# Optimization experiments

Measured on AMD Instinct MI355X. Metric: run time of the kernel, lower is better.

The kernel has to match this reference:

```python
import jax, jax.numpy as jnp
import numpy as np

H = 16
N_JOBS = 1000000
N_MACH = 500000
NEG = -1e8

PARAM_SHAPES = [("jW1",(H,H)),("jb1",(H,)),("jW2",(H,H)),("jb2",(H,)),
                ("mW1",(H,H)),("mb1",(H,)),("mW2",(H,H)),("mb2",(H,)),
                ("aj_Wq",(H,H)),("aj_bq",(H,)),("aj_Wr",(H,H)),("aj_V",(H,)),
                ("am_Wq",(H,H)),("am_bq",(H,)),("am_Wr",(H,H)),("am_V",(H,)),
                ("ja_Wq",(H,H)),("ja_bq",(H,)),("ja_Wr",(H,H)),("ja_V",(H,)),
                ("ma_Wq",(H,H)),("ma_bq",(H,)),("ma_Wr",(H,H)),("ma_V",(H,)),
                ("g1W",(H,3*H)),("g1b",(H,)),("g2W",(H,3*H)),("g2b",(H,)),
                ("last_j",(H,))]

def setup_inputs() -> dict:
    key = jax.random.key(0)
    inp = {}
    inp["jobs"] = jax.random.normal(jax.random.fold_in(key, 0), (N_JOBS, H), dtype=jnp.float32)
    inp["machines"] = jax.random.normal(jax.random.fold_in(key, 1), (N_MACH, H), dtype=jnp.float32)
    inp["alloc_jobs_mask"] = jax.random.randint(jax.random.fold_in(key, 2), (N_JOBS,), 0, 2) > 0
    for i, (name, shape) in enumerate(PARAM_SHAPES):
        inp[name] = jax.random.normal(jax.random.fold_in(key, 10 + i), shape, dtype=jnp.float32) * 0.05
    return inp

def _emb(x, W1, b1, W2, b2):
    # custom_embedding: two tanh MLP layers (torch Linear: x @ W.T + b)
    h = jnp.tanh(x @ W1.T + b1)
    return jnp.tanh(h @ W2.T + b2)

def _att_logits(q, ref, Wq, bq, Wr, V):
    # Bahdanau additive attention: tanh(W_q q + W_r ref) @ V -> [S]
    return jnp.tanh((q @ Wq.T + bq) + ref @ Wr.T) @ V

def _query_att(q, ref, Wq, bq, Wr, V):
    # Attention with use_softmax=True followed by weighted sum over ref
    w = jax.nn.softmax(_att_logits(q, ref, Wq, bq, Wr, V))
    return w @ ref  # [H]

def reference(jobs, machines, alloc_jobs_mask,
              jW1, jb1, jW2, jb2, mW1, mb1, mW2, mb2,
              aj_Wq, aj_bq, aj_Wr, aj_V, am_Wq, am_bq, am_Wr, am_V,
              ja_Wq, ja_bq, ja_Wr, ja_V, ma_Wq, ma_bq, ma_Wr, ma_V,
              g1W, g1b, g2W, g2b, last_j):
    E_j = _emb(jobs, jW1, jb1, jW2, jb2)        # [Sj, H]
    E_m = _emb(machines, mW1, mb1, mW2, mb2)    # [Sm, H]

    # glimpse 1 conditioned on last_j
    g_j1 = _query_att(last_j, E_j, aj_Wq, aj_bq, aj_Wr, aj_V)
    g_m1 = _query_att(last_j, E_m, am_Wq, am_bq, am_Wr, am_V)
    g1 = jnp.tanh(jnp.concatenate([last_j, g_j1, g_m1]) @ g1W.T + g1b)

    # job pointer logits + invalid-action masking
    j_logits = _att_logits(g1, E_j, ja_Wq, ja_bq, ja_Wr, ja_V)
    j_logits = jnp.where(alloc_jobs_mask, j_logits, NEG)
    sel_j = jnp.argmax(j_logits)
    e_js = E_j[sel_j]

    # glimpse 2 conditioned on selected job embedding
    g_j2 = _query_att(e_js, E_j, aj_Wq, aj_bq, aj_Wr, aj_V)
    g_m2 = _query_att(e_js, E_m, am_Wq, am_bq, am_Wr, am_V)
    g2 = jnp.tanh(jnp.concatenate([e_js, g_j2, g_m2]) @ g2W.T + g2b)

    m_logits = _att_logits(g2, E_m, ma_Wq, ma_bq, ma_Wr, ma_V)
    sel_m = jnp.argmax(m_logits)

    logpas = jax.nn.log_softmax(j_logits)[sel_j] + jax.nn.log_softmax(m_logits)[sel_m]
    return sel_j, sel_m, logpas
```

## Files before the change

kernel.cpp:

```cpp
#include <hip/hip_runtime.h>
#include <cstddef>
#include <cstdint>


constexpr int NJ = 1000000;
constexpr int NM = 500000;
constexpr float NEGV = -1e8f;

constexpr int BLK = 256;
constexpr int ROWS_PER_BLK = 512;
constexpr int GB_J2 = (NJ + ROWS_PER_BLK - 1) / ROWS_PER_BLK;
constexpr int GB_M2 = (NM + ROWS_PER_BLK - 1) / ROWS_PER_BLK;
constexpr int GB_TOT2 = GB_J2 + GB_M2;
constexpr int EBLK = ROWS_PER_BLK * 16;

constexpr int S_QKJA = 0;
constexpr int S_QK2J = 16;
constexpr int S_QK2M = 32;
constexpr int S_EJS  = 48;
constexpr int S_QKMA = 64;
constexpr int S_LOGPJ = 80;
constexpr int S_SELJ  = 81;
constexpr int P1J = 128;
constexpr int P1M = P1J + GB_J2 * 17;
constexpr int P2V = P1M + GB_M2 * 17;
constexpr int P2I = P2V + GB_J2;
constexpr int P2L = P2I + GB_J2;
constexpr size_t E_OFF = 65536;
static_assert(P2L + GB_J2 <= (int)E_OFF, "partials overflow into E cache");

typedef float v2f __attribute__((ext_vector_type(2)));

struct Params {
    const float *jobs, *machines;
    const int *mask;
    const float *jW1, *jb1, *jW2, *jb2;
    const float *mW1, *mb1, *mW2, *mb2;
    const float *aj_Wq, *aj_bq, *aj_Wr, *aj_V;
    const float *am_Wq, *am_bq, *am_Wr, *am_V;
    const float *ja_Wq, *ja_bq, *ja_Wr, *ja_V;
    const float *ma_Wq, *ma_bq, *ma_Wr, *ma_V;
    const float *g1W, *g1b, *g2W, *g2b, *last_j;
    float *S;
    float *Ej, *Em;
    float *out;
};


__device__ __forceinline__ float fast_tanh(float x) {
    float e = __builtin_amdgcn_exp2f(x * 2.8853900817779268f);
    float r = __builtin_amdgcn_rcpf(e + 1.0f);
    return fmaf(-2.0f, r, 1.0f);
}

__device__ __forceinline__ v2f vbc(float a) { v2f r; r.x = a; r.y = a; return r; }

__device__ __forceinline__ v2f vfma(float w, v2f b, v2f c) {
    return __builtin_elementwise_fma(vbc(w), b, c);
}
__device__ __forceinline__ v2f vfma2(v2f a, v2f b, v2f c) {
    return __builtin_elementwise_fma(a, b, c);
}
__device__ __forceinline__ v2f vtanh(v2f a) {
    v2f r; r.x = fast_tanh(a.x); r.y = fast_tanh(a.y); return r;
}

__device__ __forceinline__ void load16(const float* __restrict__ X, size_t r, float (&x)[16]) {
    const float4* p4 = reinterpret_cast<const float4*>(X) + r * 4;
    float4 a = p4[0], b = p4[1], c = p4[2], d = p4[3];
    x[0]=a.x; x[1]=a.y; x[2]=a.z; x[3]=a.w;
    x[4]=b.x; x[5]=b.y; x[6]=b.z; x[7]=b.w;
    x[8]=c.x; x[9]=c.y; x[10]=c.z; x[11]=c.w;
    x[12]=d.x; x[13]=d.y; x[14]=d.z; x[15]=d.w;
}

__device__ __forceinline__ void load16_v2(const float* __restrict__ X, size_t rA, size_t rB,
                                          v2f (&x)[16]) {
    float a[16], b[16];
    load16(X, rA, a);
    load16(X, rB, b);
#pragma unroll
    for (int k = 0; k < 16; ++k) { x[k].x = a[k]; x[k].y = b[k]; }
}

__device__ __forceinline__ void ecache_store(float* __restrict__ Eb, int t, const v2f (&e)[16]) {
    float4* p4 = reinterpret_cast<float4*>(Eb);
#pragma unroll
    for (int kp = 0; kp < 8; ++kp)
        p4[kp * 256 + t] = make_float4(e[2*kp].x, e[2*kp].y, e[2*kp+1].x, e[2*kp+1].y);
}
__device__ __forceinline__ void ecache_load(const float* __restrict__ Eb, int t, v2f (&e)[16]) {
    const float4* p4 = reinterpret_cast<const float4*>(Eb);
#pragma unroll
    for (int kp = 0; kp < 8; ++kp) {
        float4 q = p4[kp * 256 + t];
        e[2*kp].x = q.x;   e[2*kp].y = q.y;
        e[2*kp+1].x = q.z; e[2*kp+1].y = q.w;
    }
}

__device__ __forceinline__ void emb16_v2(const v2f (&x)[16],
                                         const float* __restrict__ W1, const float* __restrict__ b1,
                                         const float* __restrict__ W2, const float* __restrict__ b2,
                                         v2f (&e)[16]) {
    v2f h[16];
#pragma unroll
    for (int i = 0; i < 16; ++i) {
        v2f a = vbc(b1[i]);
#pragma unroll
        for (int k = 0; k < 16; ++k) a = vfma(W1[i * 16 + k], x[k], a);
        h[i] = vtanh(a);
    }
#pragma unroll
    for (int i = 0; i < 16; ++i) {
        v2f a = vbc(b2[i]);
#pragma unroll
        for (int k = 0; k < 16; ++k) a = vfma(W2[i * 16 + k], h[k], a);
        e[i] = vtanh(a);
    }
}

__device__ __forceinline__ v2f att_logit_v2(const v2f (&e)[16], const float (&qk)[16],
                                            const float* __restrict__ Wr,
                                            const float* __restrict__ V) {
    v2f acc = vbc(0.0f);
#pragma unroll
    for (int i = 0; i < 16; ++i) {
        v2f r = vbc(qk[i]);
#pragma unroll
        for (int k = 0; k < 16; ++k) r = vfma(Wr[i * 16 + k], e[k], r);
        acc = vfma2(vbc(V[i]), vtanh(r), acc);
    }
    return acc;
}

__device__ __forceinline__ float wave_reduce_sum(float v) {
#pragma unroll
    for (int off = 32; off > 0; off >>= 1) v += __shfl_xor(v, off, 64);
    return v;
}

__device__ __forceinline__ void wave_reduce_argmax(float &v, int &idx) {
#pragma unroll
    for (int off = 32; off > 0; off >>= 1) {
        float ov = __shfl_xor(v, off, 64);
        int oi = __shfl_xor(idx, off, 64);
        if (ov > v || (ov == v && oi < idx)) { v = ov; idx = oi; }
    }
}

__device__ __forceinline__ float block_sum(float v) {
    __shared__ float sm[4];
    v = wave_reduce_sum(v);
    __syncthreads();
    if ((threadIdx.x & 63) == 0) sm[threadIdx.x >> 6] = v;
    __syncthreads();
    return sm[0] + sm[1] + sm[2] + sm[3];
}

__device__ __forceinline__ void block_argmax(float &v, int &i) {
    __shared__ float sv[4];
    __shared__ int si[4];
    wave_reduce_argmax(v, i);
    __syncthreads();
    if ((threadIdx.x & 63) == 0) { sv[threadIdx.x >> 6] = v; si[threadIdx.x >> 6] = i; }
    __syncthreads();
    float bv = sv[0]; int bi = si[0];
#pragma unroll
    for (int k = 1; k < 4; ++k)
        if (sv[k] > bv || (sv[k] == bv && si[k] < bi)) { bv = sv[k]; bi = si[k]; }
    v = bv; i = bi;
}

__device__ __forceinline__ void block_sum17(float l, float (&s)[16], float* dst) {
    l = wave_reduce_sum(l);
#pragma unroll
    for (int i = 0; i < 16; ++i) s[i] = wave_reduce_sum(s[i]);
    __shared__ float red[4][17];
    int w = threadIdx.x >> 6, ln = threadIdx.x & 63;
    __syncthreads();
    if (ln == 0) {
        red[w][0] = l;
#pragma unroll
        for (int i = 0; i < 16; ++i) red[w][1 + i] = s[i];
    }
    __syncthreads();
    if (threadIdx.x < 17)
        dst[threadIdx.x] = red[0][threadIdx.x] + red[1][threadIdx.x] + red[2][threadIdx.x] + red[3][threadIdx.x];
}

template <bool CACHE>
__global__ __launch_bounds__(BLK) void k_emb_g1(Params p) {
    const bool isJob = blockIdx.x < GB_J2;
    const float* X  = isJob ? p.jobs : p.machines;
    const float* W1 = isJob ? p.jW1 : p.mW1;
    const float* b1 = isJob ? p.jb1 : p.mb1;
    const float* W2 = isJob ? p.jW2 : p.mW2;
    const float* b2 = isJob ? p.jb2 : p.mb2;
    const float* Wr = isJob ? p.aj_Wr : p.am_Wr;
    const float* V  = isJob ? p.aj_V  : p.am_V;
    float* E = isJob ? p.Ej : p.Em;
    const int n  = isJob ? NJ : NM;
    const int b0 = isJob ? (int)blockIdx.x : (int)blockIdx.x - GB_J2;

    __shared__ float qks[16];
    if (threadIdx.x < 16) {
        const float* Wq = isJob ? p.aj_Wq : p.am_Wq;
        const float* bq = isJob ? p.aj_bq : p.am_bq;
        const int i = threadIdx.x;
        float a = bq[i];
#pragma unroll
        for (int k = 0; k < 16; ++k) a = fmaf(Wq[i * 16 + k], p.last_j[k], a);
        qks[i] = a;
    }
    __syncthreads();
    float qk[16];
#pragma unroll
    for (int i = 0; i < 16; ++i) qk[i] = qks[i];

    const int r0 = b0 * ROWS_PER_BLK + 2 * (int)threadIdx.x;
    const int r1 = r0 + 1;
    const bool v0 = r0 < n, v1 = r1 < n;
    const size_t a0 = (size_t)(v0 ? r0 : 0);
    const size_t a1 = (size_t)(v1 ? r1 : 0);

    v2f x[16], e[16];
    load16_v2(X, a0, a1, x);
    emb16_v2(x, W1, b1, W2, b2, e);
    if (CACHE) ecache_store(E + (size_t)b0 * EBLK, (int)threadIdx.x, e);
    v2f lg = att_logit_v2(e, qk, Wr, V);
    float pw0 = v0 ? __expf(lg.x) : 0.0f;
    float pw1 = v1 ? __expf(lg.y) : 0.0f;
    float l = pw0 + pw1, s[16];
#pragma unroll
    for (int i = 0; i < 16; ++i) s[i] = fmaf(pw0, e[i].x, pw1 * e[i].y);

    block_sum17(l, s, p.S + (isJob ? P1J : P1M) + (size_t)b0 * 17);
}

__global__ __launch_bounds__(BLK) void k_combine_g(Params p, int phase) {
    const float* PJ = p.S + P1J;
    const float* PM = p.S + P1M;
    float lJ = 0.0f, lM = 0.0f, sJ[16], sM[16];
#pragma unroll
    for (int c = 0; c < 16; ++c) { sJ[c] = 0.0f; sM[c] = 0.0f; }
    for (int i = threadIdx.x; i < GB_J2; i += BLK) {
        lJ += PJ[i * 17];
#pragma unroll
        for (int c = 0; c < 16; ++c) sJ[c] += PJ[i * 17 + 1 + c];
    }
    for (int i = threadIdx.x; i < GB_M2; i += BLK) {
        lM += PM[i * 17];
#pragma unroll
        for (int c = 0; c < 16; ++c) sM[c] += PM[i * 17 + 1 + c];
    }
    __shared__ float totJ[17], totM[17];
    block_sum17(lJ, sJ, totJ);
    block_sum17(lM, sM, totM);
    __syncthreads();

    __shared__ float cb[48], gbuf[16];
    if (threadIdx.x < 16) {
        int i = threadIdx.x;
        cb[i]      = phase ? p.S[S_EJS + i] : p.last_j[i];
        cb[16 + i] = totJ[1 + i] / totJ[0];
        cb[32 + i] = totM[1 + i] / totM[0];
    }
    __syncthreads();
    const float* gW  = phase ? p.g2W : p.g1W;
    const float* gbv = phase ? p.g2b : p.g1b;
    if (threadIdx.x < 16) {
        int i = threadIdx.x;
        float a = gbv[i];
#pragma unroll
        for (int k = 0; k < 48; ++k) a = fmaf(gW[i * 48 + k], cb[k], a);
        gbuf[i] = fast_tanh(a);
    }
    __syncthreads();
    const float* Wq = phase ? p.ma_Wq : p.ja_Wq;
    const float* bq = phase ? p.ma_bq : p.ja_bq;
    const int off = phase ? S_QKMA : S_QKJA;
    if (threadIdx.x < 16) {
        int i = threadIdx.x;
        float a = bq[i];
#pragma unroll
        for (int k = 0; k < 16; ++k) a = fmaf(Wq[i * 16 + k], gbuf[k], a);
        p.S[off + i] = a;
    }
}

template <bool CACHE>
__global__ __launch_bounds__(BLK) void k_jlogits(Params p) {
    float qk[16];
#pragma unroll
    for (int i = 0; i < 16; ++i) qk[i] = p.S[S_QKJA + i];

    const int r0 = blockIdx.x * ROWS_PER_BLK + 2 * (int)threadIdx.x;
    const int r1 = r0 + 1;
    const bool v0 = r0 < NJ, v1 = r1 < NJ;
    const size_t a0 = (size_t)(v0 ? r0 : 0);
    const size_t a1 = (size_t)(v1 ? r1 : 0);

    v2f e[16];
    if (CACHE) {
        ecache_load(p.Ej + (size_t)blockIdx.x * EBLK, (int)threadIdx.x, e);
    } else {
        v2f x[16];
        load16_v2(p.jobs, a0, a1, x);
        emb16_v2(x, p.jW1, p.jb1, p.jW2, p.jb2, e);
    }
    v2f lg = att_logit_v2(e, qk, p.ja_Wr, p.ja_V);
    const bool m0 = v0 && (p.mask[a0] != 0);
    const bool m1 = v1 && (p.mask[a1] != 0);
    float l = (m0 ? __expf(lg.x) : 0.0f) + (m1 ? __expf(lg.y) : 0.0f);
    float am0 = m0 ? lg.x : NEGV - 1.0f;
    float am1 = m1 ? lg.y : NEGV - 1.0f;
    float best;
    int bi;
    if (am0 >= am1) { best = am0; bi = r0; }
    else            { best = am1; bi = r1; }

    l = wave_reduce_sum(l);
    wave_reduce_argmax(best, bi);
    __shared__ float rl[4], rv[4];
    __shared__ int ri[4];
    int w = threadIdx.x >> 6, ln = threadIdx.x & 63;
    if (ln == 0) { rl[w] = l; rv[w] = best; ri[w] = bi; }
    __syncthreads();
    if (threadIdx.x == 0) {
        float L = rl[0] + rl[1] + rl[2] + rl[3];
        float v = rv[0]; int i = ri[0];
#pragma unroll
        for (int k = 1; k < 4; ++k)
            if (rv[k] > v || (rv[k] == v && ri[k] < i)) { v = rv[k]; i = ri[k]; }
        p.S[P2V + blockIdx.x] = v;
        p.S[P2I + blockIdx.x] = (float)i;
        p.S[P2L + blockIdx.x] = L;
    }
}

__global__ __launch_bounds__(BLK) void k_combine2(Params p) {
    float v = -3.4e38f; int vi = 0x7fffffff; float l = 0.0f;
    for (int i = threadIdx.x; i < GB_J2; i += BLK) {
        float pv = p.S[P2V + i];
        int pi = (int)p.S[P2I + i];
        if (pv > v || (pv == v && pi < vi)) { v = pv; vi = pi; }
        l += p.S[P2L + i];
    }
    l = block_sum(l);
    block_argmax(v, vi);
    const int sel = vi;

    __shared__ float xb[16], hb[16], eb[16];
    if (threadIdx.x < 16) xb[threadIdx.x] = p.jobs[(size_t)sel * 16 + threadIdx.x];
    __syncthreads();
    if (threadIdx.x < 16) {
        int i = threadIdx.x;
        float a = p.jb1[i];
#pragma unroll
        for (int k = 0; k < 16; ++k) a = fmaf(p.jW1[i * 16 + k], xb[k], a);
        hb[i] = fast_tanh(a);
    }
    __syncthreads();
    if (threadIdx.x < 16) {
        int i = threadIdx.x;
        float a = p.jb2[i];
#pragma unroll
        for (int k = 0; k < 16; ++k) a = fmaf(p.jW2[i * 16 + k], hb[k], a);
        float e = fast_tanh(a);
        eb[i] = e;
        p.S[S_EJS + i] = e;
    }
    __syncthreads();
    if (threadIdx.x < 16) {
        int i = threadIdx.x;
        float a1 = p.aj_bq[i], a2 = p.am_bq[i];
#pragma unroll
        for (int k = 0; k < 16; ++k) {
            a1 = fmaf(p.aj_Wq[i * 16 + k], eb[k], a1);
            a2 = fmaf(p.am_Wq[i * 16 + k], eb[k], a2);
        }
        p.S[S_QK2J + i] = a1;
        p.S[S_QK2M + i] = a2;
    }
    if (threadIdx.x == 0) {
        p.S[S_LOGPJ] = v - logf(l);
        p.S[S_SELJ] = (float)sel;
    }
}

template <bool CACHE>
__global__ __launch_bounds__(BLK) void k_glimpse2(Params p) {
    const bool isJob = blockIdx.x < GB_J2;
    const float* Wr = isJob ? p.aj_Wr : p.am_Wr;
    const float* V  = isJob ? p.aj_V  : p.am_V;
    const float* E  = isJob ? p.Ej : p.Em;
    const float* X  = isJob ? p.jobs : p.machines;
    const float* W1 = isJob ? p.jW1 : p.mW1;
    const float* b1 = isJob ? p.jb1 : p.mb1;
    const float* W2 = isJob ? p.jW2 : p.mW2;
    const float* b2 = isJob ? p.jb2 : p.mb2;
    const int n  = isJob ? NJ : NM;
    const int b0 = isJob ? (int)blockIdx.x : (int)blockIdx.x - GB_J2;
    const int qoff = isJob ? S_QK2J : S_QK2M;

    float qk[16];
#pragma unroll
    for (int i = 0; i < 16; ++i) qk[i] = p.S[qoff + i];

    const int r0 = b0 * ROWS_PER_BLK + 2 * (int)threadIdx.x;
    const int r1 = r0 + 1;
    const bool v0 = r0 < n, v1 = r1 < n;
    const size_t a0 = (size_t)(v0 ? r0 : 0);
    const size_t a1 = (size_t)(v1 ? r1 : 0);

    v2f e[16];
    if (CACHE) {
        ecache_load(E + (size_t)b0 * EBLK, (int)threadIdx.x, e);
    } else {
        v2f x[16];
        load16_v2(X, a0, a1, x);
        emb16_v2(x, W1, b1, W2, b2, e);
    }
    v2f lg = att_logit_v2(e, qk, Wr, V);
    float pw0 = v0 ? __expf(lg.x) : 0.0f;
    float pw1 = v1 ? __expf(lg.y) : 0.0f;
    float l = pw0 + pw1, s[16];
#pragma unroll
    for (int i = 0; i < 16; ++i) s[i] = fmaf(pw0, e[i].x, pw1 * e[i].y);

    block_sum17(l, s, p.S + (isJob ? P1J : P1M) + (size_t)b0 * 17);
}

template <bool CACHE>
__global__ __launch_bounds__(BLK) void k_mlogits(Params p) {
    float qk[16];
#pragma unroll
    for (int i = 0; i < 16; ++i) qk[i] = p.S[S_QKMA + i];

    const int r0 = blockIdx.x * ROWS_PER_BLK + 2 * (int)threadIdx.x;
    const int r1 = r0 + 1;
    const bool v0 = r0 < NM, v1 = r1 < NM;
    const size_t a0 = (size_t)(v0 ? r0 : 0);
    const size_t a1 = (size_t)(v1 ? r1 : 0);

    v2f e[16];
    if (CACHE) {
        ecache_load(p.Em + (size_t)blockIdx.x * EBLK, (int)threadIdx.x, e);
    } else {
        v2f x[16];
        load16_v2(p.machines, a0, a1, x);
        emb16_v2(x, p.mW1, p.mb1, p.mW2, p.mb2, e);
    }
    v2f lg = att_logit_v2(e, qk, p.ma_Wr, p.ma_V);
    float l = (v0 ? __expf(lg.x) : 0.0f) + (v1 ? __expf(lg.y) : 0.0f);
    float am0 = v0 ? lg.x : -3.4e38f;
    float am1 = v1 ? lg.y : -3.4e38f;
    float best;
    int bi;
    if (am0 >= am1) { best = am0; bi = r0; }
    else            { best = am1; bi = r1; }

    l = wave_reduce_sum(l);
    wave_reduce_argmax(best, bi);
    __shared__ float rl[4], rv[4];
    __shared__ int ri[4];
    int w = threadIdx.x >> 6, ln = threadIdx.x & 63;
    if (ln == 0) { rl[w] = l; rv[w] = best; ri[w] = bi; }
    __syncthreads();
    if (threadIdx.x == 0) {
        float L = rl[0] + rl[1] + rl[2] + rl[3];
        float v = rv[0]; int i = ri[0];
#pragma unroll
        for (int k = 1; k < 4; ++k)
            if (rv[k] > v || (rv[k] == v && ri[k] < i)) { v = rv[k]; i = ri[k]; }
        p.S[P2V + blockIdx.x] = v;
        p.S[P2I + blockIdx.x] = (float)i;
        p.S[P2L + blockIdx.x] = L;
    }
}

__global__ __launch_bounds__(BLK) void k_combine4(Params p) {
    float v = -3.4e38f; int vi = 0x7fffffff; float l = 0.0f;
    for (int i = threadIdx.x; i < GB_M2; i += BLK) {
        float pv = p.S[P2V + i];
        int pi = (int)p.S[P2I + i];
        if (pv > v || (pv == v && pi < vi)) { v = pv; vi = pi; }
        l += p.S[P2L + i];
    }
    l = block_sum(l);
    block_argmax(v, vi);
    if (threadIdx.x == 0) {
        p.out[0] = p.S[S_SELJ];
        p.out[1] = (float)vi;
        p.out[2] = p.S[S_LOGPJ] + (v - logf(l));
    }
}

extern "C" void kernel_launch(void* const* d_in, const int* in_sizes, int n_in,
                              void* d_out, int out_size, void* d_ws, size_t ws_size,
                              hipStream_t stream) {
    Params p;
    p.jobs     = (const float*)d_in[0];
    p.machines = (const float*)d_in[1];
    p.mask     = (const int*)d_in[2];
    p.jW1 = (const float*)d_in[3];  p.jb1 = (const float*)d_in[4];
    p.jW2 = (const float*)d_in[5];  p.jb2 = (const float*)d_in[6];
    p.mW1 = (const float*)d_in[7];  p.mb1 = (const float*)d_in[8];
    p.mW2 = (const float*)d_in[9];  p.mb2 = (const float*)d_in[10];
    p.aj_Wq = (const float*)d_in[11]; p.aj_bq = (const float*)d_in[12];
    p.aj_Wr = (const float*)d_in[13]; p.aj_V  = (const float*)d_in[14];
    p.am_Wq = (const float*)d_in[15]; p.am_bq = (const float*)d_in[16];
    p.am_Wr = (const float*)d_in[17]; p.am_V  = (const float*)d_in[18];
    p.ja_Wq = (const float*)d_in[19]; p.ja_bq = (const float*)d_in[20];
    p.ja_Wr = (const float*)d_in[21]; p.ja_V  = (const float*)d_in[22];
    p.ma_Wq = (const float*)d_in[23]; p.ma_bq = (const float*)d_in[24];
    p.ma_Wr = (const float*)d_in[25]; p.ma_V  = (const float*)d_in[26];
    p.g1W = (const float*)d_in[27]; p.g1b = (const float*)d_in[28];
    p.g2W = (const float*)d_in[29]; p.g2b = (const float*)d_in[30];
    p.last_j = (const float*)d_in[31];
    p.S = (float*)d_ws;
    p.Ej = (float*)d_ws + E_OFF;
    p.Em = p.Ej + (size_t)GB_J2 * EBLK;
    p.out = (float*)d_out;

    const size_t needed = (E_OFF + (size_t)GB_TOT2 * EBLK) * sizeof(float);
    const bool cache = ws_size >= needed;

    if (cache) {
        k_emb_g1<true><<<GB_TOT2, BLK, 0, stream>>>(p);
        k_combine_g<<<1, BLK, 0, stream>>>(p, 0);
        k_jlogits<true><<<GB_J2, BLK, 0, stream>>>(p);
        k_combine2<<<1, BLK, 0, stream>>>(p);
        k_glimpse2<true><<<GB_TOT2, BLK, 0, stream>>>(p);
        k_combine_g<<<1, BLK, 0, stream>>>(p, 1);
        k_mlogits<true><<<GB_M2, BLK, 0, stream>>>(p);
        k_combine4<<<1, BLK, 0, stream>>>(p);
    } else {
        k_emb_g1<false><<<GB_TOT2, BLK, 0, stream>>>(p);
        k_combine_g<<<1, BLK, 0, stream>>>(p, 0);
        k_jlogits<false><<<GB_J2, BLK, 0, stream>>>(p);
        k_combine2<<<1, BLK, 0, stream>>>(p);
        k_glimpse2<false><<<GB_TOT2, BLK, 0, stream>>>(p);
        k_combine_g<<<1, BLK, 0, stream>>>(p, 1);
        k_mlogits<false><<<GB_M2, BLK, 0, stream>>>(p);
        k_combine4<<<1, BLK, 0, stream>>>(p);
    }
}
```

Measured before the change: 304.7 us.

## Recompute embeddings in every sweep instead of caching them, use transposed block reduction

Drops the workspace cache of the job and machine embeddings. Each of the four sweeps now reloads the raw inputs and recomputes the two-layer tanh MLP, trading extra ALU work for less memory traffic: the raw 16-float rows are the same size as the cached ones, but the large cache write in the first sweep goes away. The 17-value block reduction now uses a transpose-style butterfly, so each lane ends up holding one channel sum and far fewer shuffles are issued. The mask is read with a single int2 load, and validity is checked per pair, which assumes the row counts are even.

```diff
diff --git a/kernel.cpp b/kernel.cpp
--- a/kernel.cpp
+++ b/kernel.cpp
@@ -12,7 +12,6 @@
 constexpr int GB_J2 = (NJ + ROWS_PER_BLK - 1) / ROWS_PER_BLK;
 constexpr int GB_M2 = (NM + ROWS_PER_BLK - 1) / ROWS_PER_BLK;
 constexpr int GB_TOT2 = GB_J2 + GB_M2;
-constexpr int EBLK = ROWS_PER_BLK * 16;
 
 constexpr int S_QKJA = 0;
 constexpr int S_QK2J = 16;
@@ -26,8 +25,6 @@
 constexpr int P2V = P1M + GB_M2 * 17;
 constexpr int P2I = P2V + GB_J2;
 constexpr int P2L = P2I + GB_J2;
-constexpr size_t E_OFF = 65536;
-static_assert(P2L + GB_J2 <= (int)E_OFF, "partials overflow into E cache");
 
 typedef float v2f __attribute__((ext_vector_type(2)));
 
@@ -42,7 +39,6 @@
     const float *ma_Wq, *ma_bq, *ma_Wr, *ma_V;
     const float *g1W, *g1b, *g2W, *g2b, *last_j;
     float *S;
-    float *Ej, *Em;
     float *out;
 };
 
@@ -83,22 +79,6 @@
     for (int k = 0; k < 16; ++k) { x[k].x = a[k]; x[k].y = b[k]; }
 }
 
-__device__ __forceinline__ void ecache_store(float* __restrict__ Eb, int t, const v2f (&e)[16]) {
-    float4* p4 = reinterpret_cast<float4*>(Eb);
-#pragma unroll
-    for (int kp = 0; kp < 8; ++kp)
-        p4[kp * 256 + t] = make_float4(e[2*kp].x, e[2*kp].y, e[2*kp+1].x, e[2*kp+1].y);
-}
-__device__ __forceinline__ void ecache_load(const float* __restrict__ Eb, int t, v2f (&e)[16]) {
-    const float4* p4 = reinterpret_cast<const float4*>(Eb);
-#pragma unroll
-    for (int kp = 0; kp < 8; ++kp) {
-        float4 q = p4[kp * 256 + t];
-        e[2*kp].x = q.x;   e[2*kp].y = q.y;
-        e[2*kp+1].x = q.z; e[2*kp+1].y = q.w;
-    }
-}
-
 __device__ __forceinline__ void emb16_v2(const v2f (&x)[16],
                                          const float* __restrict__ W1, const float* __restrict__ b1,
                                          const float* __restrict__ W2, const float* __restrict__ b2,
@@ -172,25 +152,52 @@
     v = bv; i = bi;
 }
 
-__device__ __forceinline__ void block_sum17(float l, float (&s)[16], float* dst) {
-    l = wave_reduce_sum(l);
-#pragma unroll
-    for (int i = 0; i < 16; ++i) s[i] = wave_reduce_sum(s[i]);
+__device__ __forceinline__ void block_sum17(float l, const float (&s)[16], float* dst) {
+    const int lane = threadIdx.x & 63;
+    float c[8];
+#pragma unroll
+    for (int j = 0; j < 8; ++j) {
+        const bool hi = lane & 1;
+        float t = __shfl_xor(hi ? s[j] : s[j + 8], 1, 64);
+        c[j] = (hi ? s[j + 8] : s[j]) + t;
+    }
+    float d[4];
+#pragma unroll
+    for (int j = 0; j < 4; ++j) {
+        const bool hi = lane & 2;
+        float t = __shfl_xor(hi ? c[j] : c[j + 4], 2, 64);
+        d[j] = (hi ? c[j + 4] : c[j]) + t;
+    }
+    float e2[2];
+#pragma unroll
+    for (int j = 0; j < 2; ++j) {
+        const bool hi = lane & 4;
+        float t = __shfl_xor(hi ? d[j] : d[j + 2], 4, 64);
+        e2[j] = (hi ? d[j + 2] : d[j]) + t;
+    }
+    float f;
+    {
+        const bool hi = lane & 8;
+        float t = __shfl_xor(hi ? e2[0] : e2[1], 8, 64);
+        f = (hi ? e2[1] : e2[0]) + t;
+    }
+    f += __shfl_xor(f, 16, 64);
+    f += __shfl_xor(f, 32, 64);
+#pragma unroll
+    for (int off = 32; off > 0; off >>= 1) l += __shfl_xor(l, off, 64);
+
+    const int idx = ((lane & 1) << 3) | ((lane & 2) << 1) | ((lane & 4) >> 1) | ((lane & 8) >> 3);
     __shared__ float red[4][17];
-    int w = threadIdx.x >> 6, ln = threadIdx.x & 63;
-    __syncthreads();
-    if (ln == 0) {
-        red[w][0] = l;
-#pragma unroll
-        for (int i = 0; i < 16; ++i) red[w][1 + i] = s[i];
-    }
+    const int w = threadIdx.x >> 6;
+    __syncthreads();
+    if (lane < 16) red[w][1 + idx] = f;
+    if (lane == 0) red[w][0] = l;
     __syncthreads();
     if (threadIdx.x < 17)
         dst[threadIdx.x] = red[0][threadIdx.x] + red[1][threadIdx.x] + red[2][threadIdx.x] + red[3][threadIdx.x];
 }
 
-template <bool CACHE>
-__global__ __launch_bounds__(BLK) void k_emb_g1(Params p) {
+__global__ __launch_bounds__(BLK) void k_sweepA(Params p) {
     const bool isJob = blockIdx.x < GB_J2;
     const float* X  = isJob ? p.jobs : p.machines;
     const float* W1 = isJob ? p.jW1 : p.mW1;
@@ -199,7 +206,6 @@
     const float* b2 = isJob ? p.jb2 : p.mb2;
     const float* Wr = isJob ? p.aj_Wr : p.am_Wr;
     const float* V  = isJob ? p.aj_V  : p.am_V;
-    float* E = isJob ? p.Ej : p.Em;
     const int n  = isJob ? NJ : NM;
     const int b0 = isJob ? (int)blockIdx.x : (int)blockIdx.x - GB_J2;
 
@@ -219,18 +225,16 @@
     for (int i = 0; i < 16; ++i) qk[i] = qks[i];
 
     const int r0 = b0 * ROWS_PER_BLK + 2 * (int)threadIdx.x;
-    const int r1 = r0 + 1;
-    const bool v0 = r0 < n, v1 = r1 < n;
-    const size_t a0 = (size_t)(v0 ? r0 : 0);
-    const size_t a1 = (size_t)(v1 ? r1 : 0);
+    const bool v = r0 < n;
+    const size_t a0 = (size_t)(v ? r0 : 0);
+    const size_t a1 = a0 + (v ? 1 : 0);
 
     v2f x[16], e[16];
     load16_v2(X, a0, a1, x);
     emb16_v2(x, W1, b1, W2, b2, e);
-    if (CACHE) ecache_store(E + (size_t)b0 * EBLK, (int)threadIdx.x, e);
     v2f lg = att_logit_v2(e, qk, Wr, V);
-    float pw0 = v0 ? __expf(lg.x) : 0.0f;
-    float pw1 = v1 ? __expf(lg.y) : 0.0f;
+    float pw0 = v ? __expf(lg.x) : 0.0f;
+    float pw1 = v ? __expf(lg.y) : 0.0f;
     float l = pw0 + pw1, s[16];
 #pragma unroll
     for (int i = 0; i < 16; ++i) s[i] = fmaf(pw0, e[i].x, pw1 * e[i].y);
@@ -289,36 +293,32 @@
     }
 }
 
-template <bool CACHE>
-__global__ __launch_bounds__(BLK) void k_jlogits(Params p) {
+__global__ __launch_bounds__(BLK) void k_sweepB(Params p) {
     float qk[16];
 #pragma unroll
     for (int i = 0; i < 16; ++i) qk[i] = p.S[S_QKJA + i];
 
     const int r0 = blockIdx.x * ROWS_PER_BLK + 2 * (int)threadIdx.x;
-    const int r1 = r0 + 1;
-    const bool v0 = r0 < NJ, v1 = r1 < NJ;
-    const size_t a0 = (size_t)(v0 ? r0 : 0);
-    const size_t a1 = (size_t)(v1 ? r1 : 0);
-
-    v2f e[16];
-    if (CACHE) {
-        ecache_load(p.Ej + (size_t)blockIdx.x * EBLK, (int)threadIdx.x, e);
-    } else {
-        v2f x[16];
-        load16_v2(p.jobs, a0, a1, x);
-        emb16_v2(x, p.jW1, p.jb1, p.jW2, p.jb2, e);
-    }
+    const bool v = r0 < NJ;
+    const size_t a0 = (size_t)(v ? r0 : 0);
+    const size_t a1 = a0 + (v ? 1 : 0);
+
+    v2f x[16], e[16];
+    load16_v2(p.jobs, a0, a1, x);
+    emb16_v2(x, p.jW1, p.jb1, p.jW2, p.jb2, e);
     v2f lg = att_logit_v2(e, qk, p.ja_Wr, p.ja_V);
-    const bool m0 = v0 && (p.mask[a0] != 0);
-    const bool m1 = v1 && (p.mask[a1] != 0);
+
+    int2 mq = make_int2(0, 0);
+    if (v) mq = *reinterpret_cast<const int2*>(p.mask + r0);
+    const bool m0 = v && (mq.x != 0);
+    const bool m1 = v && (mq.y != 0);
     float l = (m0 ? __expf(lg.x) : 0.0f) + (m1 ? __expf(lg.y) : 0.0f);
     float am0 = m0 ? lg.x : NEGV - 1.0f;
     float am1 = m1 ? lg.y : NEGV - 1.0f;
     float best;
     int bi;
     if (am0 >= am1) { best = am0; bi = r0; }
-    else            { best = am1; bi = r1; }
+    else            { best = am1; bi = r0 + 1; }
 
     l = wave_reduce_sum(l);
     wave_reduce_argmax(best, bi);
@@ -329,11 +329,11 @@
     __syncthreads();
     if (threadIdx.x == 0) {
         float L = rl[0] + rl[1] + rl[2] + rl[3];
-        float v = rv[0]; int i = ri[0];
+        float vv = rv[0]; int i = ri[0];
 #pragma unroll
         for (int k = 1; k < 4; ++k)
-            if (rv[k] > v || (rv[k] == v && ri[k] < i)) { v = rv[k]; i = ri[k]; }
-        p.S[P2V + blockIdx.x] = v;
+            if (rv[k] > vv || (rv[k] == vv && ri[k] < i)) { vv = rv[k]; i = ri[k]; }
+        p.S[P2V + blockIdx.x] = vv;
         p.S[P2I + blockIdx.x] = (float)i;
         p.S[P2L + blockIdx.x] = L;
     }
@@ -389,17 +389,15 @@
     }
 }
 
-template <bool CACHE>
-__global__ __launch_bounds__(BLK) void k_glimpse2(Params p) {
+__global__ __launch_bounds__(BLK) void k_sweepC(Params p) {
     const bool isJob = blockIdx.x < GB_J2;
-    const float* Wr = isJob ? p.aj_Wr : p.am_Wr;
-    const float* V  = isJob ? p.aj_V  : p.am_V;
-    const float* E  = isJob ? p.Ej : p.Em;
     const float* X  = isJob ? p.jobs : p.machines;
     const float* W1 = isJob ? p.jW1 : p.mW1;
     const float* b1 = isJob ? p.jb1 : p.mb1;
     const float* W2 = isJob ? p.jW2 : p.mW2;
     const float* b2 = isJob ? p.jb2 : p.mb2;
+    const float* Wr = isJob ? p.aj_Wr : p.am_Wr;
+    const float* V  = isJob ? p.aj_V  : p.am_V;
     const int n  = isJob ? NJ : NM;
     const int b0 = isJob ? (int)blockIdx.x : (int)blockIdx.x - GB_J2;
     const int qoff = isJob ? S_QK2J : S_QK2M;
@@ -409,22 +407,16 @@
     for (int i = 0; i < 16; ++i) qk[i] = p.S[qoff + i];
 
     const int r0 = b0 * ROWS_PER_BLK + 2 * (int)threadIdx.x;
-    const int r1 = r0 + 1;
-    const bool v0 = r0 < n, v1 = r1 < n;
-    const size_t a0 = (size_t)(v0 ? r0 : 0);
-    const size_t a1 = (size_t)(v1 ? r1 : 0);
-
-    v2f e[16];
-    if (CACHE) {
-        ecache_load(E + (size_t)b0 * EBLK, (int)threadIdx.x, e);
-    } else {
-        v2f x[16];
-        load16_v2(X, a0, a1, x);
-        emb16_v2(x, W1, b1, W2, b2, e);
-    }
+    const bool v = r0 < n;
+    const size_t a0 = (size_t)(v ? r0 : 0);
+    const size_t a1 = a0 + (v ? 1 : 0);
+
+    v2f x[16], e[16];
+    load16_v2(X, a0, a1, x);
+    emb16_v2(x, W1, b1, W2, b2, e);
     v2f lg = att_logit_v2(e, qk, Wr, V);
-    float pw0 = v0 ? __expf(lg.x) : 0.0f;
-    float pw1 = v1 ? __expf(lg.y) : 0.0f;
+    float pw0 = v ? __expf(lg.x) : 0.0f;
+    float pw1 = v ? __expf(lg.y) : 0.0f;
     float l = pw0 + pw1, s[16];
 #pragma unroll
     for (int i = 0; i < 16; ++i) s[i] = fmaf(pw0, e[i].x, pw1 * e[i].y);
@@ -432,34 +424,27 @@
     block_sum17(l, s, p.S + (isJob ? P1J : P1M) + (size_t)b0 * 17);
 }
 
-template <bool CACHE>
-__global__ __launch_bounds__(BLK) void k_mlogits(Params p) {
+__global__ __launch_bounds__(BLK) void k_sweepD(Params p) {
     float qk[16];
 #pragma unroll
     for (int i = 0; i < 16; ++i) qk[i] = p.S[S_QKMA + i];
 
     const int r0 = blockIdx.x * ROWS_PER_BLK + 2 * (int)threadIdx.x;
-    const int r1 = r0 + 1;
-    const bool v0 = r0 < NM, v1 = r1 < NM;
-    const size_t a0 = (size_t)(v0 ? r0 : 0);
-    const size_t a1 = (size_t)(v1 ? r1 : 0);
-
-    v2f e[16];
-    if (CACHE) {
-        ecache_load(p.Em + (size_t)blockIdx.x * EBLK, (int)threadIdx.x, e);
-    } else {
-        v2f x[16];
-        load16_v2(p.machines, a0, a1, x);
-        emb16_v2(x, p.mW1, p.mb1, p.mW2, p.mb2, e);
-    }
+    const bool v = r0 < NM;
+    const size_t a0 = (size_t)(v ? r0 : 0);
+    const size_t a1 = a0 + (v ? 1 : 0);
+
+    v2f x[16], e[16];
+    load16_v2(p.machines, a0, a1, x);
+    emb16_v2(x, p.mW1, p.mb1, p.mW2, p.mb2, e);
     v2f lg = att_logit_v2(e, qk, p.ma_Wr, p.ma_V);
-    float l = (v0 ? __expf(lg.x) : 0.0f) + (v1 ? __expf(lg.y) : 0.0f);
-    float am0 = v0 ? lg.x : -3.4e38f;
-    float am1 = v1 ? lg.y : -3.4e38f;
+    float l = (v ? __expf(lg.x) : 0.0f) + (v ? __expf(lg.y) : 0.0f);
+    float am0 = v ? lg.x : -3.4e38f;
+    float am1 = v ? lg.y : -3.4e38f;
     float best;
     int bi;
     if (am0 >= am1) { best = am0; bi = r0; }
-    else            { best = am1; bi = r1; }
+    else            { best = am1; bi = r0 + 1; }
 
     l = wave_reduce_sum(l);
     wave_reduce_argmax(best, bi);
@@ -470,11 +455,11 @@
     __syncthreads();
     if (threadIdx.x == 0) {
         float L = rl[0] + rl[1] + rl[2] + rl[3];
-        float v = rv[0]; int i = ri[0];
+        float vv = rv[0]; int i = ri[0];
 #pragma unroll
         for (int k = 1; k < 4; ++k)
-            if (rv[k] > v || (rv[k] == v && ri[k] < i)) { v = rv[k]; i = ri[k]; }
-        p.S[P2V + blockIdx.x] = v;
+            if (rv[k] > vv || (rv[k] == vv && ri[k] < i)) { vv = rv[k]; i = ri[k]; }
+        p.S[P2V + blockIdx.x] = vv;
         p.S[P2I + blockIdx.x] = (float)i;
         p.S[P2L + blockIdx.x] = L;
     }
@@ -520,30 +505,14 @@
     p.g2W = (const float*)d_in[29]; p.g2b = (const float*)d_in[30];
     p.last_j = (const float*)d_in[31];
     p.S = (float*)d_ws;
-    p.Ej = (float*)d_ws + E_OFF;
-    p.Em = p.Ej + (size_t)GB_J2 * EBLK;
     p.out = (float*)d_out;
 
-    const size_t needed = (E_OFF + (size_t)GB_TOT2 * EBLK) * sizeof(float);
-    const bool cache = ws_size >= needed;
-
-    if (cache) {
-        k_emb_g1<true><<<GB_TOT2, BLK, 0, stream>>>(p);
-        k_combine_g<<<1, BLK, 0, stream>>>(p, 0);
-        k_jlogits<true><<<GB_J2, BLK, 0, stream>>>(p);
-        k_combine2<<<1, BLK, 0, stream>>>(p);
-        k_glimpse2<true><<<GB_TOT2, BLK, 0, stream>>>(p);
-        k_combine_g<<<1, BLK, 0, stream>>>(p, 1);
-        k_mlogits<true><<<GB_M2, BLK, 0, stream>>>(p);
-        k_combine4<<<1, BLK, 0, stream>>>(p);
-    } else {
-        k_emb_g1<false><<<GB_TOT2, BLK, 0, stream>>>(p);
-        k_combine_g<<<1, BLK, 0, stream>>>(p, 0);
-        k_jlogits<false><<<GB_J2, BLK, 0, stream>>>(p);
-        k_combine2<<<1, BLK, 0, stream>>>(p);
-        k_glimpse2<false><<<GB_TOT2, BLK, 0, stream>>>(p);
-        k_combine_g<<<1, BLK, 0, stream>>>(p, 1);
-        k_mlogits<false><<<GB_M2, BLK, 0, stream>>>(p);
-        k_combine4<<<1, BLK, 0, stream>>>(p);
-    }
-}
+    k_sweepA<<<GB_TOT2, BLK, 0, stream>>>(p);
+    k_combine_g<<<1, BLK, 0, stream>>>(p, 0);
+    k_sweepB<<<GB_J2, BLK, 0, stream>>>(p);
+    k_combine2<<<1, BLK, 0, stream>>>(p);
+    k_sweepC<<<GB_TOT2, BLK, 0, stream>>>(p);
+    k_combine_g<<<1, BLK, 0, stream>>>(p, 1);
+    k_sweepD<<<GB_M2, BLK, 0, stream>>>(p);
+    k_combine4<<<1, BLK, 0, stream>>>(p);
+}
```

Result: slower. 336.0 us (+10.3%).
